# Optimization experiments

Hardware: AMD Instinct MI355X
Metric: run time of the kernel (lower is better)

Reference implementation:

```python
import jax, jax.numpy as jnp
import numpy as np

DIM = 1024
NUM_HEADS = 16
NUM_KV_HEADS = 2
HEAD_DIM = DIM // NUM_HEADS          # 64
REPEATS = NUM_HEADS // NUM_KV_HEADS  # 8
WINDOW = 256
HALF = WINDOW // 2                   # 128
BATCH, SEQ = 2, 2048


def setup_inputs() -> dict:
    key = jax.random.key(0)
    ks = jax.random.split(key, 9)
    sc = 1.0 / np.sqrt(DIM)
    return {
        "x":  jax.random.normal(ks[0], (BATCH, SEQ, DIM), jnp.float32),
        "Wq": jax.random.normal(ks[1], (DIM, NUM_HEADS * HEAD_DIM), jnp.float32) * sc,
        "bq": jax.random.normal(ks[2], (NUM_HEADS * HEAD_DIM,), jnp.float32) * 0.01,
        "Wk": jax.random.normal(ks[3], (DIM, NUM_KV_HEADS * HEAD_DIM), jnp.float32) * sc,
        "bk": jax.random.normal(ks[4], (NUM_KV_HEADS * HEAD_DIM,), jnp.float32) * 0.01,
        "Wv": jax.random.normal(ks[5], (DIM, NUM_KV_HEADS * HEAD_DIM), jnp.float32) * sc,
        "bv": jax.random.normal(ks[6], (NUM_KV_HEADS * HEAD_DIM,), jnp.float32) * 0.01,
        "Wo": jax.random.normal(ks[7], (DIM, DIM), jnp.float32) * sc,
        "bo": jax.random.normal(ks[8], (DIM,), jnp.float32) * 0.01,
    }


def reference(x, Wq, bq, Wk, bk, Wv, bv, Wo, bo):
    # Training-path GQA sliding-window attention (faithful to the torch module):
    #  - K/V zero-padded by HALF on each side of the sequence; window of size
    #    WINDOW centered on each query position (unfold with step 1).
    #  - NOTE (faithful): the original code builds mask = tril(ones)[-1], which is
    #    an all-ones row, so masked_fill is a no-op -> NO causal mask inside the
    #    window; padded positions contribute score 0 (not -inf) to the softmax.
    #  - NOTE (faithful): the training path does NOT scale scores by 1/sqrt(d).
    b, s, _ = x.shape
    q = (x @ Wq + bq).reshape(b, s, NUM_HEADS, HEAD_DIM).transpose(0, 2, 1, 3)      # [b,H,s,d]
    k = (x @ Wk + bk).reshape(b, s, NUM_KV_HEADS, HEAD_DIM).transpose(0, 2, 1, 3)   # [b,G,s,d]
    v = (x @ Wv + bv).reshape(b, s, NUM_KV_HEADS, HEAD_DIM).transpose(0, 2, 1, 3)

    kp = jnp.pad(k, ((0, 0), (0, 0), (HALF, HALF), (0, 0)))  # [b,G,s+W,d]
    vp = jnp.pad(v, ((0, 0), (0, 0), (HALF, HALF), (0, 0)))

    # window gather indices: window i covers padded positions [i, i+W)
    idx = jnp.arange(s)[:, None] + jnp.arange(WINDOW)[None, :]  # [s,W]
    k_win = kp[:, :, idx]  # [b,G,s,W,d]  (gather at kv-head granularity, not H)
    v_win = vp[:, :, idx]

    # group query heads by kv head: head h -> kv group h // REPEATS
    qg = q.reshape(b, NUM_KV_HEADS, REPEATS, s, HEAD_DIM)        # [b,G,r,s,d]
    scores = jnp.einsum('bgrsd,bgswd->bgrsw', qg, k_win)         # no scaling (faithful)
    probs = jax.nn.softmax(scores, axis=-1)
    out = jnp.einsum('bgrsw,bgswd->bgrsd', probs, v_win)         # [b,G,r,s,d]

    out = out.reshape(b, NUM_HEADS, s, HEAD_DIM).transpose(0, 2, 1, 3).reshape(b, s, DIM)
    return out @ Wo + bo
```

## Files before the change

### kernel.cpp

```cpp
#include <hip/hip_runtime.h>
#include <hip/hip_fp16.h>

typedef _Float16 h16;
typedef __attribute__((ext_vector_type(4))) _Float16 h16x4;
typedef __attribute__((ext_vector_type(8))) _Float16 h16x8;
typedef __attribute__((ext_vector_type(4))) float f32x4;
typedef __attribute__((ext_vector_type(16))) float f32x16;
typedef __attribute__((ext_vector_type(4))) unsigned u32x4;

#define DIM   1024
#define SEQ   2048
#define NKV   2
#define HD    64
#define HALFW 128
#define NQKV  1280
#define SPAD  2304
#define KPS   (SPAD*HD)
#define LOG2E 1.4426950408889634f

__global__ void preprocess_kernel(const float* __restrict__ x,
                                  const float* __restrict__ bq,
                                  const float* __restrict__ bk,
                                  const float* __restrict__ bv,
                                  const float* __restrict__ Wq,
                                  const float* __restrict__ Wk,
                                  const float* __restrict__ Wv,
                                  const float* __restrict__ Wo,
                                  h16* __restrict__ xh, float* __restrict__ bqkv,
                                  h16* __restrict__ wqkvt, h16* __restrict__ wot,
                                  h16* __restrict__ kpad, h16* __restrict__ vtpad)
{
    __shared__ float tile[32][33];
    const int tid = threadIdx.x;
    const int blk = blockIdx.x;
    if (blk < 2048) {
        int i = blk * 256 + tid;
        size_t base = (size_t)i * 8;
        float4 a = *(const float4*)(x + base);
        float4 b = *(const float4*)(x + base + 4);
        h16x8 o = { (h16)a.x,(h16)a.y,(h16)a.z,(h16)a.w,
                    (h16)b.x,(h16)b.y,(h16)b.z,(h16)b.w };
        *(h16x8*)(xh + base) = o;
        if (i < NQKV) {
            float v = (i < DIM) ? bq[i] * LOG2E
                                : (i < DIM+128 ? bk[i-DIM] : bv[i-DIM-128]);
            bqkv[i] = v;
        }
        return;
    }
    if (blk >= 4352) {
        int idx = (blk - 4352) * 256 + tid;
        h16x8 z8 = {};
        h16* dstb = (idx < 16384) ? kpad : vtpad;
        int i2 = idx & 16383;
        int bg = i2 >> 12, j = i2 & 4095;
        if (j < 2048) {
            size_t off;
            if (idx < 16384) {
                off = (j < 1024) ? (size_t)j*8 : (size_t)2176*HD + (size_t)(j-1024)*8;
            } else {
                int d = j >> 5, r = j & 31;
                off = (size_t)d*SPAD + ((r & 16) ? 2176 : 0) + (size_t)(r & 15)*8;
            }
            *(h16x8*)(dstb + (size_t)bg*KPS + off) = z8;
        }
        return;
    }
    const int tx = tid & 31, ty = tid >> 5;
    if (blk < 2048 + 1280) {
        int bid = blk - 2048;
        int n0 = (bid % 40) * 32, k0 = (bid / 40) * 32;
        const float* src; int ldn, noff; float scl;
        if (n0 < DIM)          { src = Wq; ldn = DIM; noff = n0; scl = LOG2E; }
        else if (n0 < DIM+128) { src = Wk; ldn = 128; noff = n0 - DIM; scl = 1.f; }
        else                   { src = Wv; ldn = 128; noff = n0 - DIM - 128; scl = 1.f; }
#pragma unroll
        for (int i = 0; i < 4; ++i)
            tile[ty + 8*i][tx] = src[(size_t)(k0 + ty + 8*i)*ldn + noff + tx] * scl;
        __syncthreads();
#pragma unroll
        for (int i = 0; i < 4; ++i)
            wqkvt[(size_t)(n0 + ty + 8*i)*DIM + k0 + tx] = (h16)tile[tx][ty + 8*i];
    } else {
        int bid = blk - 3328;
        int n0 = (bid % 32) * 32, k0 = (bid / 32) * 32;
#pragma unroll
        for (int i = 0; i < 4; ++i)
            tile[ty + 8*i][tx] = Wo[(size_t)(k0 + ty + 8*i)*DIM + n0 + tx];
        __syncthreads();
#pragma unroll
        for (int i = 0; i < 4; ++i)
            wot[(size_t)(n0 + ty + 8*i)*DIM + k0 + tx] = (h16)tile[tx][ty + 8*i];
    }
}

__global__ void vtrans_kernel(const h16* __restrict__ v, h16* __restrict__ vt)
{
    __shared__ h16 tile[32][33];
    const int s0 = blockIdx.x * 32, d0 = blockIdx.y * 32, bg = blockIdx.z;
    const h16* src = v  + (size_t)bg * SEQ * HD;
    h16*       dst = vt + (size_t)bg * KPS;
    const int tx = threadIdx.x & 31, ty = threadIdx.x >> 5;
#pragma unroll
    for (int i = 0; i < 4; ++i)
        tile[ty + 8*i][tx] = src[(size_t)(s0 + ty + 8*i)*HD + d0 + tx];
    __syncthreads();
#pragma unroll
    for (int i = 0; i < 4; ++i)
        dst[(size_t)(d0 + ty + 8*i)*SPAD + HALFW + s0 + tx] = tile[tx][ty + 8*i];
}

template<int MODE>
__global__ __launch_bounds__(256, 3)
void gemm_kernel(const h16* __restrict__ A, const h16* __restrict__ Bt,
                 const float* __restrict__ bias,
                 h16* __restrict__ qo, h16* __restrict__ ko, h16* __restrict__ vo,
                 float* __restrict__ co, int K, int nx)
{
    __shared__ __align__(16) h16 As[2][128*64];
    __shared__ __align__(16) h16 Bs[2][64*64];
    const int nwg = gridDim.x, bid = blockIdx.x;
    const int wg = (bid & 7) * (nwg >> 3) + (bid >> 3);
    const int m0 = (wg / nx) * 128, n0 = (wg % nx) * 64;
    const int tid = threadIdx.x, lane = tid & 63, wid = tid >> 6;
    const int wr = wid >> 1, wc = wid & 1;
    f32x4 acc[4][2] = {};

    auto stage = [&](int buf, int kk) {
#pragma unroll
        for (int i = 0; i < 4; ++i) {
            int slot = i*256 + tid;
            int row = slot >> 3;
            int scol = ((slot & 7) ^ (row & 7)) * 8;
            __builtin_amdgcn_global_load_lds(
                (const __attribute__((address_space(1))) void*)(A + (size_t)(m0 + row)*K + kk + scol),
                (__attribute__((address_space(3))) void*)(&As[buf][slot*8]), 16, 0, 0);
        }
#pragma unroll
        for (int i = 0; i < 2; ++i) {
            int slot = i*256 + tid;
            int row = slot >> 3;
            int scol = ((slot & 7) ^ (row & 7)) * 8;
            __builtin_amdgcn_global_load_lds(
                (const __attribute__((address_space(1))) void*)(Bt + (size_t)(n0 + row)*K + kk + scol),
                (__attribute__((address_space(3))) void*)(&Bs[buf][slot*8]), 16, 0, 0);
        }
    };
    auto compute = [&](int buf) {
#pragma unroll
        for (int k2 = 0; k2 < 2; ++k2) {
            h16x8 a[4], b[2];
#pragma unroll
            for (int mi = 0; mi < 4; ++mi) {
                int row = wr*64 + mi*16 + (lane & 15);
                int cc = (k2*4 + (lane >> 4)) ^ (row & 7);
                a[mi] = *(const h16x8*)(&As[buf][row*64 + cc*8]);
            }
#pragma unroll
            for (int ni = 0; ni < 2; ++ni) {
                int row = wc*32 + ni*16 + (lane & 15);
                int cc = (k2*4 + (lane >> 4)) ^ (row & 7);
                b[ni] = *(const h16x8*)(&Bs[buf][row*64 + cc*8]);
            }
#pragma unroll
            for (int mi = 0; mi < 4; ++mi)
#pragma unroll
                for (int ni = 0; ni < 2; ++ni)
                    acc[mi][ni] = __builtin_amdgcn_mfma_f32_16x16x32_f16(a[mi], b[ni], acc[mi][ni], 0, 0, 0);
        }
    };

    const int ns = K >> 6;
    stage(0, 0);
    int cur = 0;
    for (int i = 0; i < ns; ++i) {
        if (i < ns-1) {
            stage(cur ^ 1, (i+1) << 6);
            asm volatile("s_waitcnt vmcnt(6)" ::: "memory");
        } else {
            asm volatile("s_waitcnt vmcnt(0)" ::: "memory");
        }
        __builtin_amdgcn_s_barrier();
        __builtin_amdgcn_sched_barrier(0);
        compute(cur);
        if (i < ns-1) {
            __builtin_amdgcn_s_barrier();
            __builtin_amdgcn_sched_barrier(0);
        }
        cur ^= 1;
    }

#pragma unroll
    for (int ni = 0; ni < 2; ++ni) {
        int n = n0 + wc*32 + ni*16 + (lane & 15);
        float bv = bias[n];
#pragma unroll
        for (int mi = 0; mi < 4; ++mi) {
            int mb = m0 + wr*64 + mi*16 + (lane >> 4)*4;
#pragma unroll
            for (int r = 0; r < 4; ++r) {
                int m = mb + r;
                float v = acc[mi][ni][r] + bv;
                if (MODE == 1) {
                    co[(size_t)m*DIM + n] = v;
                } else {
                    h16 hv = (h16)v;
                    if (n < DIM) {
                        qo[(size_t)m*DIM + n] = hv;
                    } else {
                        int nn = n - DIM;
                        int bi2 = m >> 11, s = m & 2047;
                        int g = (nn & 127) >> 6, d = nn & 63;
                        if (nn < 128)
                            ko[((size_t)(bi2*NKV + g)*SPAD + s + HALFW)*HD + d] = hv;
                        else
                            vo[(((size_t)(bi2*NKV + g))*SEQ + s)*HD + d] = hv;
                    }
                }
            }
        }
    }
}

__global__ __launch_bounds__(512)
void attn_kernel(const h16* __restrict__ qb, const h16* __restrict__ kpad,
                 const h16* __restrict__ vtpad, h16* __restrict__ ob)
{
    extern __shared__ char smem[];
    h16* Ks  = (h16*)smem;
    h16* Vts = (h16*)(smem + 36864);
    const int tid = threadIdx.x, lane = tid & 63, wid = tid >> 6;
    const int qt = blockIdx.x, g = blockIdx.y, bi = blockIdx.z;
    const int s0 = qt * 32;
    const h16* Kbase = kpad  + (size_t)(bi*NKV + g)*KPS + (size_t)s0*HD;
    const h16* Vbase = vtpad + (size_t)(bi*NKV + g)*KPS + s0;

    for (int slot = tid; slot < 288*8; slot += 512) {
        int row = slot >> 3, cc = slot & 7;
        h16x8 val = *(const h16x8*)(Kbase + (size_t)row*HD + cc*8);
        *(h16x8*)(Ks + row*64 + ((cc ^ (row & 7)) * 8)) = val;
    }
    for (int slot = tid; slot < 64*36; slot += 512) {
        int row = slot / 36, cc = slot - row*36;
        h16x8 val = *(const h16x8*)(Vbase + (size_t)row*SPAD + cc*8);
        *(h16x8*)(Vts + row*320 + ((cc ^ (row & 7)) * 8)) = val;
    }
    __syncthreads();

    const int h = g*8 + wid;
    const int q = lane & 31, hi2 = lane >> 5;

    h16x8 aq[4];
#pragma unroll
    for (int c = 0; c < 4; ++c)
        aq[c] = *(const h16x8*)(qb + ((size_t)(bi*SEQ + s0 + q))*DIM
                                + h*HD + c*16 + hi2*8);

    f32x16 sc[9];
    __builtin_amdgcn_s_setprio(1);
#pragma unroll
    for (int T = 0; T < 9; ++T) {
        f32x16 z = {};
#pragma unroll
        for (int c = 0; c < 4; ++c) {
            int key = T*32 + q;
            int chunk = (2*c + hi2) ^ (key & 7);
            h16x8 kf = *(const h16x8*)(Ks + key*64 + chunk*8);
            z = __builtin_amdgcn_mfma_f32_32x32x16_f16(kf, aq[c], z, 0, 0, 0);
        }
        sc[T] = z;
    }
    __builtin_amdgcn_s_setprio(0);

    float mx = -1e30f;
#pragma unroll
    for (int r = 0; r < 16; ++r) {
        int krow = (r & 3) + 8*(r >> 2) + 4*hi2;
        float v0 = (krow >= q) ? sc[0][r] : -1e30f;
        float v8 = (krow <  q) ? sc[8][r] : -1e30f;
        sc[0][r] = v0; sc[8][r] = v8;
        mx = fmaxf(mx, fmaxf(v0, v8));
    }
#pragma unroll
    for (int T = 1; T < 8; ++T)
#pragma unroll
        for (int r = 0; r < 16; ++r) mx = fmaxf(mx, sc[T][r]);
    mx = fmaxf(mx, __shfl_xor(mx, 32));
    float sum = 0.f;
#pragma unroll
    for (int T = 0; T < 9; ++T)
#pragma unroll
        for (int r = 0; r < 16; ++r) {
            float p = exp2f(sc[T][r] - mx);
            sc[T][r] = p;
            sum += p;
        }
    sum += __shfl_xor(sum, 32);
    float inv = 1.0f / sum;

    unsigned pk[72];
#pragma unroll
    for (int T = 0; T < 9; ++T)
#pragma unroll
        for (int p = 0; p < 8; ++p) {
            h16 lo = (h16)(sc[T][2*p]   * inv);
            h16 hi = (h16)(sc[T][2*p+1] * inv);
            pk[T*8+p] = (unsigned)__builtin_bit_cast(unsigned short, lo)
                      | ((unsigned)__builtin_bit_cast(unsigned short, hi) << 16);
        }

    f32x16 ao0 = {}, ao1 = {};
    const bool hb = (hi2 != 0);
    __builtin_amdgcn_s_setprio(1);
#pragma unroll
    for (int c = 0; c < 18; ++c) {
        const int base = (c >> 1)*8 + (c & 1)*4;
        unsigned D0 = pk[base], D1 = pk[base+1], D2 = pk[base+2], D3 = pk[base+3];
        unsigned X0 = __shfl_xor(D0, 32), X1 = __shfl_xor(D1, 32);
        unsigned X2 = __shfl_xor(D2, 32), X3 = __shfl_xor(D3, 32);
        u32x4 pav = { hb ? X2 : D0, hb ? X3 : D1, hb ? D2 : X0, hb ? D3 : X1 };
        h16x8 pa = __builtin_bit_cast(h16x8, pav);
#pragma unroll
        for (int dt = 0; dt < 2; ++dt) {
            int d = dt*32 + q;
            int chunk = (2*c + hi2) ^ (d & 7);
            h16x8 vb = *(const h16x8*)(Vts + d*320 + chunk*8);
            if (dt == 0) ao0 = __builtin_amdgcn_mfma_f32_32x32x16_f16(pa, vb, ao0, 0, 0, 0);
            else         ao1 = __builtin_amdgcn_mfma_f32_32x32x16_f16(pa, vb, ao1, 0, 0, 0);
        }
    }
    __builtin_amdgcn_s_setprio(0);

#pragma unroll
    for (int r = 0; r < 16; ++r) {
        int qrow = (r & 3) + 8*(r >> 2) + 4*hi2;
        size_t rowoff = ((size_t)(bi*SEQ + s0 + qrow))*DIM + h*HD;
        ob[rowoff + q]      = (h16)ao0[r];
        ob[rowoff + 32 + q] = (h16)ao1[r];
    }
}

extern "C" void kernel_launch(void* const* d_in, const int* in_sizes, int n_in,
                              void* d_out, int out_size, void* d_ws, size_t ws_size,
                              hipStream_t stream)
{
    const float* x  = (const float*)d_in[0];
    const float* Wq = (const float*)d_in[1];
    const float* bq = (const float*)d_in[2];
    const float* Wk = (const float*)d_in[3];
    const float* bk = (const float*)d_in[4];
    const float* Wv = (const float*)d_in[5];
    const float* bv = (const float*)d_in[6];
    const float* Wo = (const float*)d_in[7];
    const float* bo = (const float*)d_in[8];
    float* out = (float*)d_out;
    char* ws = (char*)d_ws;

    h16*   xh    = (h16*)(ws);
    h16*   wqkvt = (h16*)(ws + 8388608);
    h16*   wot   = (h16*)(ws + 11010048);
    float* bqkv  = (float*)(ws + 13107200);
    h16*   q_b   = (h16*)(ws + 13112320);
    h16*   k_pad = (h16*)(ws + 21500928);
    h16*   vt_pad= (h16*)(ws + 22680576);
    h16*   att_b = (h16*)(ws + 23860224);
    h16*   v_b   = att_b;

    preprocess_kernel<<<4480, 256, 0, stream>>>(x, bq, bk, bv, Wq, Wk, Wv, Wo,
                                                xh, bqkv, wqkvt, wot, k_pad, vt_pad);
    gemm_kernel<0><<<640, 256, 0, stream>>>(xh, wqkvt, bqkv,
                                            q_b, k_pad, v_b, nullptr, DIM, 20);
    vtrans_kernel<<<dim3(64, 2, 4), 256, 0, stream>>>(v_b, vt_pad);
    hipFuncSetAttribute((const void*)attn_kernel,
                        hipFuncAttributeMaxDynamicSharedMemorySize, 77824);
    attn_kernel<<<dim3(64, 2, 2), 512, 77824, stream>>>(q_b, k_pad, vt_pad, att_b);
    gemm_kernel<1><<<512, 256, 0, stream>>>(att_b, wot, bo,
                                            nullptr, nullptr, nullptr, out, DIM, 16);
}
```

Measured before the change: 72.88 us.

## Fuse V transpose into QKV GEMM epilogue and use online softmax in attention

The QKV GEMM now writes V directly in transposed, padded layout. It stages each V tile through shared memory and emits vector stores, so the separate vtrans kernel launch and its round trip through memory are gone. The attention kernel switches to an online softmax per 32-key tile, which drops the large score and probability register arrays. It also splits each KV group's 8 heads across two 256-thread blocks, doubling the grid at the cost of loading K/V into shared memory twice and adding per-tile rescale shuffles.

```diff
diff --git a/kernel.cpp b/kernel.cpp
--- a/kernel.cpp
+++ b/kernel.cpp
@@ -94,22 +94,6 @@
     }
 }
 
-__global__ void vtrans_kernel(const h16* __restrict__ v, h16* __restrict__ vt)
-{
-    __shared__ h16 tile[32][33];
-    const int s0 = blockIdx.x * 32, d0 = blockIdx.y * 32, bg = blockIdx.z;
-    const h16* src = v  + (size_t)bg * SEQ * HD;
-    h16*       dst = vt + (size_t)bg * KPS;
-    const int tx = threadIdx.x & 31, ty = threadIdx.x >> 5;
-#pragma unroll
-    for (int i = 0; i < 4; ++i)
-        tile[ty + 8*i][tx] = src[(size_t)(s0 + ty + 8*i)*HD + d0 + tx];
-    __syncthreads();
-#pragma unroll
-    for (int i = 0; i < 4; ++i)
-        dst[(size_t)(d0 + ty + 8*i)*SPAD + HALFW + s0 + tx] = tile[tx][ty + 8*i];
-}
-
 template<int MODE>
 __global__ __launch_bounds__(256, 3)
 void gemm_kernel(const h16* __restrict__ A, const h16* __restrict__ Bt,
@@ -190,6 +174,35 @@
         cur ^= 1;
     }
 
+    if (MODE == 0 && n0 >= DIM + 128) {
+        __syncthreads();
+        h16* T = &As[0][0];
+        const int g = (n0 - DIM - 128) >> 6;
+#pragma unroll
+        for (int ni = 0; ni < 2; ++ni) {
+            int nrel = wc*32 + ni*16 + (lane & 15);
+            float bv = bias[n0 + nrel];
+#pragma unroll
+            for (int mi = 0; mi < 4; ++mi) {
+                int mrel = wr*64 + mi*16 + (lane >> 4)*4;
+#pragma unroll
+                for (int r = 0; r < 4; ++r)
+                    T[nrel*136 + mrel + r] = (h16)(acc[mi][ni][r] + bv);
+            }
+        }
+        __syncthreads();
+        const int bi2 = m0 >> 11, sbase = m0 & 2047;
+        h16* dst = vo + ((size_t)(bi2*NKV + g))*KPS + HALFW + sbase;
+#pragma unroll
+        for (int i = 0; i < 4; ++i) {
+            int slot = i*256 + tid;
+            int d = slot >> 4, cc = slot & 15;
+            h16x8 val = *(const h16x8*)(T + d*136 + cc*8);
+            *(h16x8*)(dst + (size_t)d*SPAD + cc*8) = val;
+        }
+        return;
+    }
+
 #pragma unroll
     for (int ni = 0; ni < 2; ++ni) {
         int n = n0 + wc*32 + ni*16 + (lane & 15);
@@ -210,11 +223,8 @@
                     } else {
                         int nn = n - DIM;
                         int bi2 = m >> 11, s = m & 2047;
-                        int g = (nn & 127) >> 6, d = nn & 63;
-                        if (nn < 128)
-                            ko[((size_t)(bi2*NKV + g)*SPAD + s + HALFW)*HD + d] = hv;
-                        else
-                            vo[(((size_t)(bi2*NKV + g))*SEQ + s)*HD + d] = hv;
+                        int g = nn >> 6, d = nn & 63;
+                        ko[((size_t)(bi2*NKV + g)*SPAD + s + HALFW)*HD + d] = hv;
                     }
                 }
             }
@@ -222,7 +232,7 @@
     }
 }
 
-__global__ __launch_bounds__(512)
+__global__ __launch_bounds__(256, 2)
 void attn_kernel(const h16* __restrict__ qb, const h16* __restrict__ kpad,
                  const h16* __restrict__ vtpad, h16* __restrict__ ob)
 {
@@ -230,25 +240,27 @@
     h16* Ks  = (h16*)smem;
     h16* Vts = (h16*)(smem + 36864);
     const int tid = threadIdx.x, lane = tid & 63, wid = tid >> 6;
-    const int qt = blockIdx.x, g = blockIdx.y, bi = blockIdx.z;
+    const int qt = blockIdx.x, quad = blockIdx.y, bi = blockIdx.z;
+    const int g = quad >> 1;
     const int s0 = qt * 32;
     const h16* Kbase = kpad  + (size_t)(bi*NKV + g)*KPS + (size_t)s0*HD;
     const h16* Vbase = vtpad + (size_t)(bi*NKV + g)*KPS + s0;
 
-    for (int slot = tid; slot < 288*8; slot += 512) {
+    for (int slot = tid; slot < 288*8; slot += 256) {
         int row = slot >> 3, cc = slot & 7;
         h16x8 val = *(const h16x8*)(Kbase + (size_t)row*HD + cc*8);
         *(h16x8*)(Ks + row*64 + ((cc ^ (row & 7)) * 8)) = val;
     }
-    for (int slot = tid; slot < 64*36; slot += 512) {
+    for (int slot = tid; slot < 64*36; slot += 256) {
         int row = slot / 36, cc = slot - row*36;
         h16x8 val = *(const h16x8*)(Vbase + (size_t)row*SPAD + cc*8);
         *(h16x8*)(Vts + row*320 + ((cc ^ (row & 7)) * 8)) = val;
     }
     __syncthreads();
 
-    const int h = g*8 + wid;
+    const int h = quad*4 + wid;
     const int q = lane & 31, hi2 = lane >> 5;
+    const bool hb = (hi2 != 0);
 
     h16x8 aq[4];
 #pragma unroll
@@ -256,11 +268,13 @@
         aq[c] = *(const h16x8*)(qb + ((size_t)(bi*SEQ + s0 + q))*DIM
                                 + h*HD + c*16 + hi2*8);
 
-    f32x16 sc[9];
-    __builtin_amdgcn_s_setprio(1);
+    f32x16 ao0 = {}, ao1 = {};
+    float m = -1e30f, sum = 0.f;
+
 #pragma unroll
     for (int T = 0; T < 9; ++T) {
         f32x16 z = {};
+        __builtin_amdgcn_s_setprio(1);
 #pragma unroll
         for (int c = 0; c < 4; ++c) {
             int key = T*32 + q;
@@ -268,75 +282,80 @@
             h16x8 kf = *(const h16x8*)(Ks + key*64 + chunk*8);
             z = __builtin_amdgcn_mfma_f32_32x32x16_f16(kf, aq[c], z, 0, 0, 0);
         }
-        sc[T] = z;
-    }
-    __builtin_amdgcn_s_setprio(0);
-
-    float mx = -1e30f;
-#pragma unroll
-    for (int r = 0; r < 16; ++r) {
-        int krow = (r & 3) + 8*(r >> 2) + 4*hi2;
-        float v0 = (krow >= q) ? sc[0][r] : -1e30f;
-        float v8 = (krow <  q) ? sc[8][r] : -1e30f;
-        sc[0][r] = v0; sc[8][r] = v8;
-        mx = fmaxf(mx, fmaxf(v0, v8));
-    }
-#pragma unroll
-    for (int T = 1; T < 8; ++T)
-#pragma unroll
-        for (int r = 0; r < 16; ++r) mx = fmaxf(mx, sc[T][r]);
-    mx = fmaxf(mx, __shfl_xor(mx, 32));
-    float sum = 0.f;
-#pragma unroll
-    for (int T = 0; T < 9; ++T)
+        __builtin_amdgcn_s_setprio(0);
+
+        if (T == 0) {
+#pragma unroll
+            for (int r = 0; r < 16; ++r) {
+                int krow = (r & 3) + 8*(r >> 2) + 4*hi2;
+                if (krow < q) z[r] = -1e30f;
+            }
+        }
+        if (T == 8) {
+#pragma unroll
+            for (int r = 0; r < 16; ++r) {
+                int krow = (r & 3) + 8*(r >> 2) + 4*hi2;
+                if (krow >= q) z[r] = -1e30f;
+            }
+        }
+
+        float lm = z[0];
+#pragma unroll
+        for (int r = 1; r < 16; ++r) lm = fmaxf(lm, z[r]);
+        lm = fmaxf(lm, __shfl_xor(lm, 32));
+        float mn = fmaxf(m, lm);
+        float rs = exp2f(m - mn);
+        sum *= rs;
 #pragma unroll
         for (int r = 0; r < 16; ++r) {
-            float p = exp2f(sc[T][r] - mx);
-            sc[T][r] = p;
-            sum += p;
-        }
+            int qrow = (r & 3) + 8*(r >> 2) + 4*hi2;
+            float rsr = __shfl(rs, qrow);
+            ao0[r] *= rsr;
+            ao1[r] *= rsr;
+        }
+        m = mn;
+
+        unsigned pk8[8];
+#pragma unroll
+        for (int p = 0; p < 8; ++p) {
+            float p0 = exp2f(z[2*p]   - m);
+            float p1 = exp2f(z[2*p+1] - m);
+            sum += p0 + p1;
+            pk8[p] = (unsigned)__builtin_bit_cast(unsigned short, (h16)p0)
+                   | ((unsigned)__builtin_bit_cast(unsigned short, (h16)p1) << 16);
+        }
+
+        __builtin_amdgcn_s_setprio(1);
+#pragma unroll
+        for (int half = 0; half < 2; ++half) {
+            unsigned D0 = pk8[half*4+0], D1 = pk8[half*4+1];
+            unsigned D2 = pk8[half*4+2], D3 = pk8[half*4+3];
+            unsigned X0 = __shfl_xor(D0, 32), X1 = __shfl_xor(D1, 32);
+            unsigned X2 = __shfl_xor(D2, 32), X3 = __shfl_xor(D3, 32);
+            u32x4 pav = { hb ? X2 : D0, hb ? X3 : D1, hb ? D2 : X0, hb ? D3 : X1 };
+            h16x8 pa = __builtin_bit_cast(h16x8, pav);
+            const int cg = 2*T + half;
+#pragma unroll
+            for (int dt = 0; dt < 2; ++dt) {
+                int d = dt*32 + q;
+                int chunk = (2*cg + hi2) ^ (d & 7);
+                h16x8 vb = *(const h16x8*)(Vts + d*320 + chunk*8);
+                if (dt == 0) ao0 = __builtin_amdgcn_mfma_f32_32x32x16_f16(pa, vb, ao0, 0, 0, 0);
+                else         ao1 = __builtin_amdgcn_mfma_f32_32x32x16_f16(pa, vb, ao1, 0, 0, 0);
+            }
+        }
+        __builtin_amdgcn_s_setprio(0);
+    }
+
     sum += __shfl_xor(sum, 32);
     float inv = 1.0f / sum;
-
-    unsigned pk[72];
-#pragma unroll
-    for (int T = 0; T < 9; ++T)
-#pragma unroll
-        for (int p = 0; p < 8; ++p) {
-            h16 lo = (h16)(sc[T][2*p]   * inv);
-            h16 hi = (h16)(sc[T][2*p+1] * inv);
-            pk[T*8+p] = (unsigned)__builtin_bit_cast(unsigned short, lo)
-                      | ((unsigned)__builtin_bit_cast(unsigned short, hi) << 16);
-        }
-
-    f32x16 ao0 = {}, ao1 = {};
-    const bool hb = (hi2 != 0);
-    __builtin_amdgcn_s_setprio(1);
-#pragma unroll
-    for (int c = 0; c < 18; ++c) {
-        const int base = (c >> 1)*8 + (c & 1)*4;
-        unsigned D0 = pk[base], D1 = pk[base+1], D2 = pk[base+2], D3 = pk[base+3];
-        unsigned X0 = __shfl_xor(D0, 32), X1 = __shfl_xor(D1, 32);
-        unsigned X2 = __shfl_xor(D2, 32), X3 = __shfl_xor(D3, 32);
-        u32x4 pav = { hb ? X2 : D0, hb ? X3 : D1, hb ? D2 : X0, hb ? D3 : X1 };
-        h16x8 pa = __builtin_bit_cast(h16x8, pav);
-#pragma unroll
-        for (int dt = 0; dt < 2; ++dt) {
-            int d = dt*32 + q;
-            int chunk = (2*c + hi2) ^ (d & 7);
-            h16x8 vb = *(const h16x8*)(Vts + d*320 + chunk*8);
-            if (dt == 0) ao0 = __builtin_amdgcn_mfma_f32_32x32x16_f16(pa, vb, ao0, 0, 0, 0);
-            else         ao1 = __builtin_amdgcn_mfma_f32_32x32x16_f16(pa, vb, ao1, 0, 0, 0);
-        }
-    }
-    __builtin_amdgcn_s_setprio(0);
-
 #pragma unroll
     for (int r = 0; r < 16; ++r) {
         int qrow = (r & 3) + 8*(r >> 2) + 4*hi2;
+        float iq = __shfl(inv, qrow);
         size_t rowoff = ((size_t)(bi*SEQ + s0 + qrow))*DIM + h*HD;
-        ob[rowoff + q]      = (h16)ao0[r];
-        ob[rowoff + 32 + q] = (h16)ao1[r];
+        ob[rowoff + q]      = (h16)(ao0[r] * iq);
+        ob[rowoff + 32 + q] = (h16)(ao1[r] * iq);
     }
 }
 
@@ -364,16 +383,14 @@
     h16*   k_pad = (h16*)(ws + 21500928);
     h16*   vt_pad= (h16*)(ws + 22680576);
     h16*   att_b = (h16*)(ws + 23860224);
-    h16*   v_b   = att_b;
 
     preprocess_kernel<<<4480, 256, 0, stream>>>(x, bq, bk, bv, Wq, Wk, Wv, Wo,
                                                 xh, bqkv, wqkvt, wot, k_pad, vt_pad);
     gemm_kernel<0><<<640, 256, 0, stream>>>(xh, wqkvt, bqkv,
-                                            q_b, k_pad, v_b, nullptr, DIM, 20);
-    vtrans_kernel<<<dim3(64, 2, 4), 256, 0, stream>>>(v_b, vt_pad);
+                                            q_b, k_pad, vt_pad, nullptr, DIM, 20);
     hipFuncSetAttribute((const void*)attn_kernel,
                         hipFuncAttributeMaxDynamicSharedMemorySize, 77824);
-    attn_kernel<<<dim3(64, 2, 2), 512, 77824, stream>>>(q_b, k_pad, vt_pad, att_b);
+    attn_kernel<<<dim3(64, 4, 2), 256, 77824, stream>>>(q_b, k_pad, vt_pad, att_b);
     gemm_kernel<1><<<512, 256, 0, stream>>>(att_b, wot, bo,
                                             nullptr, nullptr, nullptr, out, DIM, 16);
 }
```

Result: faster. 68.33 us (-6.2%).
